# Kernel optimization log

Hardware: AMD Instinct MI355X
Metric: run time of the kernel (lower is better)

Reference implementation:

```python
import jax, jax.numpy as jnp
import numpy as np

B, S, N, D = 8, 2048, 4096, 256
MAX_W = 16  # fixed cap on span width (torch code derives it from data; padding is masked)
TINY = 1e-13  # allennlp util.masked_mean clamp


def setup_inputs() -> dict:
    key = jax.random.key(0)
    k1, k2, k3 = jax.random.split(key, 3)
    sequence_tensor = jax.random.normal(k1, (B, S, D), dtype=jnp.float32)
    starts = jax.random.randint(k2, (B, N, 1), 0, S - MAX_W)
    widths = jax.random.randint(k3, (B, N, 1), 0, MAX_W)  # width in [0, MAX_W-1]
    span_indices = jnp.concatenate([starts, starts + widths], axis=-1)  # [B,N,2], ends >= starts
    return {"sequence_tensor": sequence_tensor, "span_indices": span_indices}


def reference(sequence_tensor, span_indices):
    starts = span_indices[..., 0:1]            # [B,N,1]
    ends = span_indices[..., 1:2]              # [B,N,1]
    widths = ends - starts                     # [B,N,1]
    rng = jnp.arange(MAX_W)[None, None, :]     # [1,1,W]
    raw_idx = ends - rng                       # [B,N,W] indices counting back from end
    span_mask = ((rng <= widths) & (raw_idx >= 0)).astype(sequence_tensor.dtype)  # [B,N,W]
    idx = jnp.maximum(raw_idx, 0)              # relu(raw).long()
    batch_ids = jnp.arange(sequence_tensor.shape[0])[:, None, None]
    span_embeddings = sequence_tensor[batch_ids, idx]  # gather -> [B,N,W,D]
    summed = jnp.einsum('bnwd,bnw->bnd', span_embeddings, span_mask)
    count = jnp.maximum(jnp.sum(span_mask, axis=-1, keepdims=True), TINY)  # [B,N,1]
    return summed / count  # masked mean over span positions -> [B,N,D]
```

## Files before the change

### kernel.cpp

```cpp
#include <hip/hip_runtime.h>

#define PB 8
#define PS 2048
#define PN 4096
#define PD 256
#define CHUNK 32
#define NCH (PS / CHUNK)

typedef float f4 __attribute__((ext_vector_type(4)));

__global__ __launch_bounds__(256) void chunk_prefix_kernel(
    const float* __restrict__ seq,
    float*       __restrict__ P,
    float*       __restrict__ T)
{
    const int b = blockIdx.x & 7;
    const int c = blockIdx.x >> 3;
    const int d = threadIdx.x;

    const size_t base = ((size_t)b * PS + (size_t)c * CHUNK) * PD + (size_t)d;
    const float* sp = seq + base;
    float*       pp = P   + base;

    float run = 0.0f;
#pragma unroll
    for (int s = 0; s < CHUNK; ++s) {
        run += __builtin_nontemporal_load(sp + (size_t)s * PD);
        pp[(size_t)s * PD] = run;
    }
    T[((size_t)b * NCH + c) * PD + (size_t)d] = run;
}

__global__ __launch_bounds__(256) void span_mean_kernel(
    const float* __restrict__ P,
    const float* __restrict__ T,
    const int*   __restrict__ spans,
    float*       __restrict__ out)
{
    const int b       = blockIdx.x & 7;
    const int blk     = blockIdx.x >> 3;
    const int span_ib = (blk << 2) | (threadIdx.x >> 6);
    const int span    = (b << 12) | span_ib;
    const int lane    = threadIdx.x & 63;

    const int2 se    = ((const int2*)spans)[span];
    const int  start = __builtin_amdgcn_readfirstlane(se.x);
    const int  end   = __builtin_amdgcn_readfirstlane(se.y);
    const int  width = end - start;

    const float inv = 1.0f / (float)(width + 1);

    const int   sm = (start > 0) ? (start - 1) : 0;
    const float m0 = (start > 0) ? 1.0f : 0.0f;
    const int   cs = sm >> 5;
    const int   ce = end >> 5;
    const float mt = (ce > cs) ? 1.0f : 0.0f;

    const f4* Pb = (const f4*)(P + (size_t)b * PS * PD) + lane;
    const f4 pe = Pb[(size_t)end * 64];
    const f4 ps = Pb[(size_t)sm  * 64];
    const f4 tt = ((const f4*)(T + ((size_t)b * NCH + (size_t)cs) * PD))[lane];

    f4 acc = pe - ps * m0 + tt * mt;
    acc *= inv;

    f4* outp = (f4*)(out + (size_t)span * PD) + lane;
    __builtin_nontemporal_store(acc, outp);
}

extern "C" void kernel_launch(void* const* d_in, const int* in_sizes, int n_in,
                              void* d_out, int out_size, void* d_ws, size_t ws_size,
                              hipStream_t stream) {
    const float* seq   = (const float*)d_in[0];
    const int*   spans = (const int*)d_in[1];
    float*       out   = (float*)d_out;

    float* P = (float*)d_ws;
    float* T = P + (size_t)PB * PS * PD;

    chunk_prefix_kernel<<<dim3(PB * NCH), dim3(256), 0, stream>>>(seq, P, T);

    const int n_spans = PB * PN;
    span_mean_kernel<<<dim3(n_spans / 4), dim3(256), 0, stream>>>(P, T, spans, out);
}
```

Before: 87.09 us.

## Parallelize chunk prefix across wavefronts with LDS carry and halve chunk size

```diff
diff --git a/kernel.cpp b/kernel.cpp
--- a/kernel.cpp
+++ b/kernel.cpp
@@ -4,31 +4,55 @@
 #define PS 2048
 #define PN 4096
 #define PD 256
-#define CHUNK 32
+#define CHUNK 16
 #define NCH (PS / CHUNK)
 
 typedef float f4 __attribute__((ext_vector_type(4)));
+typedef int   i2 __attribute__((ext_vector_type(2)));
 
 __global__ __launch_bounds__(256) void chunk_prefix_kernel(
     const float* __restrict__ seq,
     float*       __restrict__ P,
     float*       __restrict__ T)
 {
-    const int b = blockIdx.x & 7;
-    const int c = blockIdx.x >> 3;
-    const int d = threadIdx.x;
+    const int b    = blockIdx.x & 7;
+    const int c    = blockIdx.x >> 3;
+    const int w    = threadIdx.x >> 6;
+    const int lane = threadIdx.x & 63;
 
-    const size_t base = ((size_t)b * PS + (size_t)c * CHUNK) * PD + (size_t)d;
-    const float* sp = seq + base;
-    float*       pp = P   + base;
+    const size_t rowbase = ((size_t)b * PS + (size_t)c * CHUNK) * PD;
+    const f4* sp = (const f4*)(seq + rowbase) + lane;
+    f4*       pp = (f4*)(P + rowbase) + lane;
 
-    float run = 0.0f;
-#pragma unroll
-    for (int s = 0; s < CHUNK; ++s) {
-        run += __builtin_nontemporal_load(sp + (size_t)s * PD);
-        pp[(size_t)s * PD] = run;
-    }
-    T[((size_t)b * NCH + c) * PD + (size_t)d] = run;
+    const int r0 = w << 2;
+    f4 v0 = __builtin_nontemporal_load(sp + (size_t)(r0 + 0) * 64);
+    f4 v1 = __builtin_nontemporal_load(sp + (size_t)(r0 + 1) * 64);
+    f4 v2 = __builtin_nontemporal_load(sp + (size_t)(r0 + 2) * 64);
+    f4 v3 = __builtin_nontemporal_load(sp + (size_t)(r0 + 3) * 64);
+    v1 += v0;
+    v2 += v1;
+    v3 += v2;
+
+    __shared__ f4 tot[4][64];
+    tot[w][lane] = v3;
+    __syncthreads();
+
+    f4 carry = (f4){0.f, 0.f, 0.f, 0.f};
+    if (w > 0) carry = tot[0][lane];
+    if (w > 1) carry += tot[1][lane];
+    if (w > 2) carry += tot[2][lane];
+
+    v0 += carry;
+    v1 += carry;
+    v2 += carry;
+    v3 += carry;
+
+    pp[(size_t)(r0 + 0) * 64] = v0;
+    pp[(size_t)(r0 + 1) * 64] = v1;
+    pp[(size_t)(r0 + 2) * 64] = v2;
+    pp[(size_t)(r0 + 3) * 64] = v3;
+    if (w == 3)
+        ((f4*)(T + ((size_t)b * NCH + c) * PD))[lane] = v3;
 }
 
 __global__ __launch_bounds__(256) void span_mean_kernel(
@@ -43,25 +67,26 @@
     const int span    = (b << 12) | span_ib;
     const int lane    = threadIdx.x & 63;
 
-    const int2 se    = ((const int2*)spans)[span];
-    const int  start = __builtin_amdgcn_readfirstlane(se.x);
-    const int  end   = __builtin_amdgcn_readfirstlane(se.y);
-    const int  width = end - start;
+    const i2  se    = __builtin_nontemporal_load((const i2*)spans + span);
+    const int start = __builtin_amdgcn_readfirstlane(se.x);
+    const int end   = __builtin_amdgcn_readfirstlane(se.y);
+    const int width = end - start;
 
     const float inv = 1.0f / (float)(width + 1);
-
-    const int   sm = (start > 0) ? (start - 1) : 0;
-    const float m0 = (start > 0) ? 1.0f : 0.0f;
-    const int   cs = sm >> 5;
-    const int   ce = end >> 5;
-    const float mt = (ce > cs) ? 1.0f : 0.0f;
+    const int   sm  = (start > 0) ? (start - 1) : 0;
+    const float m0  = (start > 0) ? 1.0f : 0.0f;
+    const int   cs  = sm >> 4;
+    const int   ce  = end >> 4;
 
     const f4* Pb = (const f4*)(P + (size_t)b * PS * PD) + lane;
     const f4 pe = Pb[(size_t)end * 64];
-    const f4 ps = Pb[(size_t)sm  * 64];
-    const f4 tt = ((const f4*)(T + ((size_t)b * NCH + (size_t)cs) * PD))[lane];
+    const f4 ps = Pb[(size_t)sm * 64];
 
-    f4 acc = pe - ps * m0 + tt * mt;
+    f4 acc = pe - ps * m0;
+    if (ce > cs) {
+        const f4 tt = ((const f4*)(T + ((size_t)b * NCH + (size_t)cs) * PD))[lane];
+        acc += tt;
+    }
     acc *= inv;
 
     f4* outp = (f4*)(out + (size_t)span * PD) + lane;
```

Result: slower. 90.26 us (+3.6%).
